# Kernel tuning notes

Measured on AMD Instinct MI355X. Metric: run time of the kernel, lower is better.

## Reference

```python
import jax, jax.numpy as jnp
import numpy as np

N_NODES = 100000
N_EDGES = 1600000
N_GRAPHS = 2000
IN_DIM = 37
HID = 128
OUT_CLS = 2


def _leconv(x, src, dst, w, W1, b1, W2, W3, b3):
    # PyG LEConv: out[i] = sum_j w_ij * (lin1(x)[i] - lin2(x)[j]) + lin3(x)[i]
    a = x @ W1 + b1          # [N, H]
    b = x @ W2               # [N, H] (lin2 has no bias)
    c = x @ W3 + b3          # [N, H]
    deg = jax.ops.segment_sum(w, dst, num_segments=N_NODES)              # [N]
    agg = jax.ops.segment_sum(w[:, None] * b[src], dst, num_segments=N_NODES)  # [N, H]
    return deg[:, None] * a - agg + c


def setup_inputs() -> dict:
    key = jax.random.key(0)
    ks = jax.random.split(key, 32)
    inp = {}
    inp["x"] = jax.random.normal(ks[0], (N_NODES, IN_DIM), dtype=jnp.float32)
    inp["edge_index"] = jax.random.randint(ks[1], (2, N_EDGES), 0, N_NODES, dtype=jnp.int64)
    inp["batch"] = jnp.sort(jax.random.randint(ks[2], (N_NODES,), 0, N_GRAPHS, dtype=jnp.int64))
    dims = [(IN_DIM, HID), (HID, HID), (HID, HID)]
    ki = 3
    for l, (di, do) in enumerate(dims):
        s = 1.0 / np.sqrt(di)
        inp[f"W1_{l}"] = jax.random.uniform(ks[ki + 0], (di, do), jnp.float32, -s, s)
        inp[f"b1_{l}"] = jax.random.uniform(ks[ki + 1], (do,), jnp.float32, -s, s)
        inp[f"W2_{l}"] = jax.random.uniform(ks[ki + 2], (di, do), jnp.float32, -s, s)
        inp[f"W3_{l}"] = jax.random.uniform(ks[ki + 3], (di, do), jnp.float32, -s, s)
        inp[f"b3_{l}"] = jax.random.uniform(ks[ki + 4], (do,), jnp.float32, -s, s)
        ki += 5
    sf = 1.0 / np.sqrt(HID)
    inp["Wf1"] = jax.random.uniform(ks[ki + 0], (HID, HID), jnp.float32, -sf, sf)
    inp["bf1"] = jax.random.uniform(ks[ki + 1], (HID,), jnp.float32, -sf, sf)
    inp["Wf2"] = jax.random.uniform(ks[ki + 2], (HID, OUT_CLS), jnp.float32, -sf, sf)
    inp["bf2"] = jax.random.uniform(ks[ki + 3], (OUT_CLS,), jnp.float32, -sf, sf)
    return inp


def reference(x, edge_index, batch,
              W1_0, b1_0, W2_0, W3_0, b3_0,
              W1_1, b1_1, W2_1, W3_1, b3_1,
              W1_2, b1_2, W2_2, W3_2, b3_2,
              Wf1, bf1, Wf2, bf2):
    src, dst = edge_index[0], edge_index[1]
    w = jnp.ones((edge_index.shape[1],), dtype=x.dtype)  # edge_weight = ones
    layers = [(W1_0, b1_0, W2_0, W3_0, b3_0),
              (W1_1, b1_1, W2_1, W3_1, b3_1),
              (W1_2, b1_2, W2_2, W3_2, b3_2)]
    h = x
    for (W1, b1, W2, W3, b3) in layers:
        h = jax.nn.relu(_leconv(h, src, dst, w, W1, b1, W2, W3, b3))
    # global mean pool per graph
    sums = jax.ops.segment_sum(h, batch, num_segments=N_GRAPHS)           # [G, H]
    cnt = jax.ops.segment_sum(jnp.ones((N_NODES,), h.dtype), batch, num_segments=N_GRAPHS)
    graph_x = sums / jnp.clip(cnt, 1.0)[:, None]
    # FFN head (Dropout is identity at inference)
    pred = jax.nn.relu(graph_x @ Wf1 + bf1) @ Wf2 + bf2                   # [G, 2]
    return pred
```

## Files before the change

### kernel.cpp

```cpp
#include <hip/hip_runtime.h>
#include <hip/hip_bf16.h>
#include <cstdint>

#define N_NODES 100000
#define N_EDGES 1600000
#define N_GRAPHS 2000
#define IN_DIM 37
#define HID 128

#define GEMM_GRID 1563
#define HIST_BLOCKS 6250
#define PACK67_BLOCKS 384
#define PREPACK_BLOCKS 96

typedef __attribute__((ext_vector_type(8))) short short8;
typedef __attribute__((ext_vector_type(4))) float f32x4;

static __device__ __forceinline__ short bf16_bits(float f) {
    __hip_bfloat16 h = __float2bfloat16(f);
    return *reinterpret_cast<short*>(&h);
}
static __device__ __forceinline__ float bf16_lo(uint32_t u) {
    uint32_t v = u << 16;
    return *reinterpret_cast<float*>(&v);
}
static __device__ __forceinline__ float bf16_hi(uint32_t u) {
    uint32_t v = u & 0xffff0000u;
    return *reinterpret_cast<float*>(&v);
}
static __device__ __forceinline__ uint32_t pack_bf16(float lo, float hi) {
    return ((uint32_t)(uint16_t)bf16_bits(hi) << 16) | (uint16_t)bf16_bits(lo);
}


struct PackArgs {
    const float* w[9];
    short* o[9];
};

static __device__ __forceinline__ void pack_one(const PackArgs& pa, int m, int r, int kin) {
    const int i = r & 7, lane = (r >> 3) & 63, t = (r >> 9) & 7, kb = r >> 12;
    const int k = kb * 32 + (lane >> 4) * 8 + i;
    const int c = t * 16 + (lane & 15);
    float v = (k < kin) ? pa.w[m][(size_t)k * HID + c] : 0.f;
    pa.o[m][r] = bf16_bits(v);
}

__global__ __launch_bounds__(256) void prepack_kernel(PackArgs pa) {
    const int idx = blockIdx.x * 256 + threadIdx.x;
    pack_one(pa, idx >> 13, idx & 8191, IN_DIM);
}


static __device__ __forceinline__ void gemm0_body(
    int blk, const float* __restrict__ x,
    const short* __restrict__ Wp1, const short* __restrict__ Wp2, const short* __restrict__ Wp3,
    const float* __restrict__ b1v, const float* __restrict__ b3v,
    short* __restrict__ D0, short* __restrict__ E0, short* __restrict__ Bb) {
    const int tid = threadIdx.x;
    const int wave = tid >> 6, lane = tid & 63;
    const int row_base = blk * 64 + wave * 16;
    const int r15 = lane & 15, kg = lane >> 4;
    int arow = row_base + r15;
    if (arow >= N_NODES) arow = N_NODES - 1;
    const float* xr = x + (size_t)arow * IN_DIM;

    f32x4 acc1[8], acc2[8], acc3[8];
    #pragma unroll
    for (int t = 0; t < 8; t++) {
        acc1[t] = (f32x4)0.f; acc2[t] = (f32x4)0.f; acc3[t] = (f32x4)0.f;
    }
    #pragma unroll
    for (int kb = 0; kb < 2; kb++) {
        short8 av;
        #pragma unroll
        for (int i = 0; i < 8; i++) {
            const int k = kb * 32 + kg * 8 + i;
            av[i] = (k < IN_DIM) ? bf16_bits(xr[k]) : (short)0;
        }
        #pragma unroll
        for (int t = 0; t < 8; t++) {
            const int widx = (kb * 8 + t) * 512 + lane * 8;
            short8 w1 = *(const short8*)(Wp1 + widx);
            short8 w2 = *(const short8*)(Wp2 + widx);
            short8 w3 = *(const short8*)(Wp3 + widx);
            acc1[t] = __builtin_amdgcn_mfma_f32_16x16x32_bf16(av, w1, acc1[t], 0, 0, 0);
            acc2[t] = __builtin_amdgcn_mfma_f32_16x16x32_bf16(av, w2, acc2[t], 0, 0, 0);
            acc3[t] = __builtin_amdgcn_mfma_f32_16x16x32_bf16(av, w3, acc3[t], 0, 0, 0);
        }
    }
    int grow[4]; bool ok[4];
    #pragma unroll
    for (int i = 0; i < 4; i++) {
        grow[i] = row_base + kg * 4 + i;
        ok[i] = grow[i] < N_NODES;
    }
    #pragma unroll
    for (int t = 0; t < 8; t++) {
        const int c = t * 16 + r15;
        const float bb1 = b1v[c], bb3 = b3v[c];
        #pragma unroll
        for (int i = 0; i < 4; i++) {
            if (ok[i]) {
                size_t o = (size_t)grow[i] * HID + c;
                D0[o] = bf16_bits(acc1[t][i] + bb1);
                E0[o] = bf16_bits(acc3[t][i] + bb3);
                Bb[o] = bf16_bits(acc2[t][i]);
            }
        }
    }
}


struct P1Args {
    const float* x;
    const int* ei;
    int* cnt; int* rank;
    const short* Wp1; const short* Wp2; const short* Wp3;
    const float* b1; const float* b3;
    short* D0; short* E0; short* Bb;
    PackArgs pa;
};

__global__ __launch_bounds__(256) void phase1_kernel(P1Args a) {
    const int b = blockIdx.x;
    if (b < GEMM_GRID) {
        gemm0_body(b, a.x, a.Wp1, a.Wp2, a.Wp3, a.b1, a.b3, a.D0, a.E0, a.Bb);
        return;
    }
    if (b < GEMM_GRID + HIST_BLOCKS) {
        const int e = (b - GEMM_GRID) * 256 + threadIdx.x;
        const int d = a.ei[N_EDGES + e];
        a.rank[e] = atomicAdd(&a.cnt[d], 1);
        return;
    }
    const int idx = (b - GEMM_GRID - HIST_BLOCKS) * 256 + threadIdx.x;
    pack_one(a.pa, 3 + (idx >> 14), idx & 16383, HID);
}


__global__ __launch_bounds__(1024) void scan_blocks(const int* __restrict__ cnt,
                                                    int* __restrict__ partial,
                                                    int* __restrict__ bsum) {
    __shared__ int ws[16];
    const int tid = threadIdx.x, lane = tid & 63, wv = tid >> 6;
    const int i = blockIdx.x * 1024 + tid;
    int v0 = (i < N_NODES) ? cnt[i] : 0;
    int v = v0;
    #pragma unroll
    for (int off = 1; off < 64; off <<= 1) {
        int n = __shfl_up(v, off, 64);
        if (lane >= off) v += n;
    }
    if (lane == 63) ws[wv] = v;
    __syncthreads();
    int woff = 0, tot = 0;
    #pragma unroll
    for (int w = 0; w < 16; w++) {
        int s = ws[w];
        if (w < wv) woff += s;
        tot += s;
    }
    if (i < N_NODES) partial[i] = woff + v - v0;
    if (tid == 0) bsum[blockIdx.x] = tot;
}

__global__ __launch_bounds__(1024) void scan_finalize(const int* __restrict__ partial,
                                                      const int* __restrict__ bsum,
                                                      const int* __restrict__ cnt,
                                                      int* __restrict__ rowptr,
                                                      float* __restrict__ degf) {
    __shared__ int off_s;
    const int tid = threadIdx.x, b = blockIdx.x;
    if (tid < 64) {
        int acc = 0;
        for (int j = tid; j < b; j += 64) acc += bsum[j];
        #pragma unroll
        for (int off = 32; off; off >>= 1) acc += __shfl_down(acc, off, 64);
        if (tid == 0) off_s = acc;
    }
    __syncthreads();
    const int i = b * 1024 + tid;
    if (i < N_NODES) {
        rowptr[i] = off_s + partial[i];
        degf[i] = (float)cnt[i];
    }
    if (b == 0 && tid == 0) rowptr[N_NODES] = N_EDGES;
}


__global__ __launch_bounds__(256) void fill_kernel(const int* __restrict__ ei,
                                                   const int* __restrict__ rank,
                                                   const int* __restrict__ rowptr,
                                                   int* __restrict__ col) {
    const int e = blockIdx.x * 256 + threadIdx.x;
    const int s = ei[e];
    const int d = ei[N_EDGES + e];
    col[rowptr[d] + rank[e]] = s;
}


static __device__ __forceinline__ void agg_edges4(const int* __restrict__ col, int s, int e,
                                                  const short* __restrict__ Bb,
                                                  int lane, int grp, int l16, float* acc) {
    for (int base = s; base < e; base += 64) {
        const int cnt = min(64, e - base);
        const int ci = base + lane;
        const int cv = col[(ci < e) ? ci : (e - 1)];
        for (int t = 0; t < cnt; t += 4) {
            const int idx = t + grp;
            const bool on = idx < cnt;
            const float w = on ? 1.f : 0.f;
            const int c = __shfl(cv, on ? idx : 0, 64);
            const uint4 u = *(const uint4*)(Bb + (size_t)c * HID + l16 * 8);
            acc[0] = fmaf(w, bf16_lo(u.x), acc[0]);
            acc[1] = fmaf(w, bf16_hi(u.x), acc[1]);
            acc[2] = fmaf(w, bf16_lo(u.y), acc[2]);
            acc[3] = fmaf(w, bf16_hi(u.y), acc[3]);
            acc[4] = fmaf(w, bf16_lo(u.z), acc[4]);
            acc[5] = fmaf(w, bf16_hi(u.z), acc[5]);
            acc[6] = fmaf(w, bf16_lo(u.w), acc[6]);
            acc[7] = fmaf(w, bf16_hi(u.w), acc[7]);
        }
    }
    #pragma unroll
    for (int j = 0; j < 8; j++) {
        acc[j] += __shfl_xor(acc[j], 16, 64);
        acc[j] += __shfl_xor(acc[j], 32, 64);
    }
}

__global__ __launch_bounds__(256) void gather0_kernel(const int* __restrict__ rowptr,
                                                      const int* __restrict__ col,
                                                      const short* __restrict__ Bb,
                                                      const short* __restrict__ D0,
                                                      const short* __restrict__ E0,
                                                      short* __restrict__ Hb) {
    const int wid = (blockIdx.x * 256 + threadIdx.x) >> 6;
    if (wid >= N_NODES) return;
    const int lane = threadIdx.x & 63, grp = lane >> 4, l16 = lane & 15;
    const int s = rowptr[wid], e = rowptr[wid + 1];
    float acc[8] = {0.f, 0.f, 0.f, 0.f, 0.f, 0.f, 0.f, 0.f};
    agg_edges4(col, s, e, Bb, lane, grp, l16, acc);
    if (grp == 0) {
        const float dg = (float)(e - s);
        const uint4 ud = *(const uint4*)(D0 + (size_t)wid * HID + l16 * 8);
        const uint4 ue = *(const uint4*)(E0 + (size_t)wid * HID + l16 * 8);
        uint4 r;
        r.x = pack_bf16(fmaxf(fmaf(dg, bf16_lo(ud.x), bf16_lo(ue.x)) - acc[0], 0.f),
                        fmaxf(fmaf(dg, bf16_hi(ud.x), bf16_hi(ue.x)) - acc[1], 0.f));
        r.y = pack_bf16(fmaxf(fmaf(dg, bf16_lo(ud.y), bf16_lo(ue.y)) - acc[2], 0.f),
                        fmaxf(fmaf(dg, bf16_hi(ud.y), bf16_hi(ue.y)) - acc[3], 0.f));
        r.z = pack_bf16(fmaxf(fmaf(dg, bf16_lo(ud.z), bf16_lo(ue.z)) - acc[4], 0.f),
                        fmaxf(fmaf(dg, bf16_hi(ud.z), bf16_hi(ue.z)) - acc[5], 0.f));
        r.w = pack_bf16(fmaxf(fmaf(dg, bf16_lo(ud.w), bf16_lo(ue.w)) - acc[6], 0.f),
                        fmaxf(fmaf(dg, bf16_hi(ud.w), bf16_hi(ue.w)) - acc[7], 0.f));
        *(uint4*)(Hb + (size_t)wid * HID + l16 * 8) = r;
    }
}

__global__ __launch_bounds__(256) void gatherL_kernel(const int* __restrict__ rowptr,
                                                      const int* __restrict__ col,
                                                      const short* __restrict__ Bb,
                                                      const short* __restrict__ OUTb,
                                                      short* __restrict__ Hb) {
    const int wid = (blockIdx.x * 256 + threadIdx.x) >> 6;
    if (wid >= N_NODES) return;
    const int lane = threadIdx.x & 63, grp = lane >> 4, l16 = lane & 15;
    const int s = rowptr[wid], e = rowptr[wid + 1];
    float acc[8] = {0.f, 0.f, 0.f, 0.f, 0.f, 0.f, 0.f, 0.f};
    agg_edges4(col, s, e, Bb, lane, grp, l16, acc);
    if (grp == 0) {
        const uint4 uo = *(const uint4*)(OUTb + (size_t)wid * HID + l16 * 8);
        uint4 r;
        r.x = pack_bf16(fmaxf(bf16_lo(uo.x) - acc[0], 0.f), fmaxf(bf16_hi(uo.x) - acc[1], 0.f));
        r.y = pack_bf16(fmaxf(bf16_lo(uo.y) - acc[2], 0.f), fmaxf(bf16_hi(uo.y) - acc[3], 0.f));
        r.z = pack_bf16(fmaxf(bf16_lo(uo.z) - acc[4], 0.f), fmaxf(bf16_hi(uo.z) - acc[5], 0.f));
        r.w = pack_bf16(fmaxf(bf16_lo(uo.w) - acc[6], 0.f), fmaxf(bf16_hi(uo.w) - acc[7], 0.f));
        *(uint4*)(Hb + (size_t)wid * HID + l16 * 8) = r;
    }
}


__global__ __launch_bounds__(256) void leconv_mfma(
    const short* __restrict__ Hb,
    const short* __restrict__ Wp1, const short* __restrict__ Wp2, const short* __restrict__ Wp3,
    const float* __restrict__ b1v, const float* __restrict__ b3v,
    const float* __restrict__ deg,
    short* __restrict__ Bb, short* __restrict__ OUTb) {
    const int tid = threadIdx.x;
    const int wave = tid >> 6, lane = tid & 63;
    const int row_base = blockIdx.x * 64 + wave * 16;
    const int r15 = lane & 15, kg = lane >> 4;
    int arow = row_base + r15;
    if (arow >= N_NODES) arow = N_NODES - 1;
    const short* aptr = Hb + (size_t)arow * HID + kg * 8;

    f32x4 acc1[8], acc2[8], acc3[8];
    #pragma unroll
    for (int t = 0; t < 8; t++) {
        acc1[t] = (f32x4)0.f; acc2[t] = (f32x4)0.f; acc3[t] = (f32x4)0.f;
    }
    #pragma unroll
    for (int kb = 0; kb < 4; kb++) {
        short8 av = *(const short8*)(aptr + kb * 32);
        #pragma unroll
        for (int t = 0; t < 8; t++) {
            const int widx = (kb * 8 + t) * 512 + lane * 8;
            short8 w1 = *(const short8*)(Wp1 + widx);
            short8 w2 = *(const short8*)(Wp2 + widx);
            short8 w3 = *(const short8*)(Wp3 + widx);
            acc1[t] = __builtin_amdgcn_mfma_f32_16x16x32_bf16(av, w1, acc1[t], 0, 0, 0);
            acc2[t] = __builtin_amdgcn_mfma_f32_16x16x32_bf16(av, w2, acc2[t], 0, 0, 0);
            acc3[t] = __builtin_amdgcn_mfma_f32_16x16x32_bf16(av, w3, acc3[t], 0, 0, 0);
        }
    }
    int grow[4]; bool ok[4]; float dg[4];
    #pragma unroll
    for (int i = 0; i < 4; i++) {
        grow[i] = row_base + kg * 4 + i;
        ok[i] = grow[i] < N_NODES;
        dg[i] = ok[i] ? deg[grow[i]] : 0.f;
    }
    #pragma unroll
    for (int t = 0; t < 8; t++) {
        const int c = t * 16 + r15;
        const float bb1 = b1v[c], bb3 = b3v[c];
        #pragma unroll
        for (int i = 0; i < 4; i++) {
            if (ok[i]) {
                size_t o = (size_t)grow[i] * HID + c;
                OUTb[o] = bf16_bits(dg[i] * (acc1[t][i] + bb1) + acc3[t][i] + bb3);
                Bb[o] = bf16_bits(acc2[t][i]);
            }
        }
    }
}


__global__ __launch_bounds__(128) void pool_ffn_kernel(const short* __restrict__ H,
                                                       const int* __restrict__ batch,
                                                       const float* __restrict__ Wf1,
                                                       const float* __restrict__ bf1,
                                                       const float* __restrict__ Wf2,
                                                       const float* __restrict__ bf2,
                                                       float* __restrict__ out) {
    const int g = blockIdx.x;
    const int t = threadIdx.x;

    int lo = 0, hi = N_NODES;
    while (lo < hi) { int mid = (lo + hi) >> 1; if (batch[mid] < g) lo = mid + 1; else hi = mid; }
    const int s = lo;
    hi = N_NODES;
    while (lo < hi) { int mid = (lo + hi) >> 1; if (batch[mid] < g + 1) lo = mid + 1; else hi = mid; }
    const int e = lo;

    float sum = 0.f;
    for (int n = s; n < e; n++) {
        short b = H[(size_t)n * HID + t];
        sum += __bfloat162float(*(__hip_bfloat16*)&b);
    }
    const float cntf = (float)(e - s);
    const float gx = sum / fmaxf(cntf, 1.f);

    __shared__ float lds[HID];
    lds[t] = gx;
    __syncthreads();

    float hsum = bf1[t];
    #pragma unroll 8
    for (int k = 0; k < HID; k++) hsum = fmaf(lds[k], Wf1[k * HID + t], hsum);
    const float hr = fmaxf(hsum, 0.f);

    float p0 = hr * Wf2[t * 2 + 0];
    float p1 = hr * Wf2[t * 2 + 1];
    #pragma unroll
    for (int off = 32; off > 0; off >>= 1) {
        p0 += __shfl_down(p0, off, 64);
        p1 += __shfl_down(p1, off, 64);
    }
    __shared__ float red[4];
    if ((t & 63) == 0) {
        red[(t >> 6) * 2 + 0] = p0;
        red[(t >> 6) * 2 + 1] = p1;
    }
    __syncthreads();
    if (t == 0) {
        out[g * 2 + 0] = red[0] + red[2] + bf2[0];
        out[g * 2 + 1] = red[1] + red[3] + bf2[1];
    }
}


extern "C" void kernel_launch(void* const* d_in, const int* in_sizes, int n_in,
                              void* d_out, int out_size, void* d_ws, size_t ws_size,
                              hipStream_t stream) {
    (void)in_sizes; (void)n_in; (void)out_size; (void)ws_size;

    const float* x     = (const float*)d_in[0];
    const int*   ei    = (const int*)d_in[1];
    const int*   batch = (const int*)d_in[2];
    const float* W[9] = {
        (const float*)d_in[3],  (const float*)d_in[5],  (const float*)d_in[6],
        (const float*)d_in[8],  (const float*)d_in[10], (const float*)d_in[11],
        (const float*)d_in[13], (const float*)d_in[15], (const float*)d_in[16]};
    const float* b1_0 = (const float*)d_in[4];
    const float* b3_0 = (const float*)d_in[7];
    const float* b1_1 = (const float*)d_in[9];
    const float* b3_1 = (const float*)d_in[12];
    const float* b1_2 = (const float*)d_in[14];
    const float* b3_2 = (const float*)d_in[17];
    const float* Wf1  = (const float*)d_in[18];
    const float* bf1  = (const float*)d_in[19];
    const float* Wf2  = (const float*)d_in[20];
    const float* bf2  = (const float*)d_in[21];
    float* out = (float*)d_out;

    char* ws = (char*)d_ws;
    size_t off = 0;
    auto alloc = [&](size_t bytes) {
        void* p = ws + off;
        off += (bytes + 255) & ~(size_t)255;
        return p;
    };
    short* D0     = (short*)alloc((size_t)N_NODES * HID * 2);
    short* E0     = (short*)alloc((size_t)N_NODES * HID * 2);
    short* Bb_A   = (short*)alloc((size_t)N_NODES * HID * 2);
    short* Bb_B   = (short*)alloc((size_t)N_NODES * HID * 2);
    short* Hb     = (short*)alloc((size_t)N_NODES * HID * 2);
    float* degf   = (float*)alloc((size_t)N_NODES * 4);
    int*   rowptr = (int*)alloc((size_t)(N_NODES + 1) * 4);
    int*   cnt    = (int*)alloc((size_t)N_NODES * 4);
    int*   col    = (int*)alloc((size_t)N_EDGES * 4);
    int*   rank   = (int*)alloc((size_t)N_EDGES * 4);
    int*   partial= (int*)alloc((size_t)N_NODES * 4);
    int*   bsum   = (int*)alloc(1024);
    short* P[9];
    for (int m = 0; m < 9; m++) P[m] = (short*)alloc(16384 * 2);

    hipMemsetAsync(cnt, 0, (size_t)N_NODES * 4, stream);

    PackArgs pa;
    for (int m = 0; m < 9; m++) { pa.w[m] = W[m]; pa.o[m] = P[m]; }

    prepack_kernel<<<PREPACK_BLOCKS, 256, 0, stream>>>(pa);

    P1Args p1{ x, ei, cnt, rank, P[0], P[1], P[2], b1_0, b3_0, D0, E0, Bb_A, pa };
    phase1_kernel<<<GEMM_GRID + HIST_BLOCKS + PACK67_BLOCKS, 256, 0, stream>>>(p1);

    const int NSB = (N_NODES + 1023) / 1024;
    scan_blocks<<<NSB, 1024, 0, stream>>>(cnt, partial, bsum);
    scan_finalize<<<NSB, 1024, 0, stream>>>(partial, bsum, cnt, rowptr, degf);

    fill_kernel<<<HIST_BLOCKS, 256, 0, stream>>>(ei, rank, rowptr, col);

    const int gather_grid = (N_NODES * 64 + 255) / 256;

    gather0_kernel<<<gather_grid, 256, 0, stream>>>(rowptr, col, Bb_A, D0, E0, Hb);
    leconv_mfma<<<GEMM_GRID, 256, 0, stream>>>(Hb, P[3], P[4], P[5], b1_1, b3_1, degf, Bb_B, E0);
    gatherL_kernel<<<gather_grid, 256, 0, stream>>>(rowptr, col, Bb_B, E0, Hb);
    leconv_mfma<<<GEMM_GRID, 256, 0, stream>>>(Hb, P[6], P[7], P[8], b1_2, b3_2, degf, Bb_A, D0);
    gatherL_kernel<<<gather_grid, 256, 0, stream>>>(rowptr, col, Bb_A, D0, Hb);

    pool_ffn_kernel<<<N_GRAPHS, 128, 0, stream>>>(Hb, batch, Wf1, bf1, Wf2, bf2, out);
}
```

Baseline: 475.3 us.

## Fuse final gather with mean-pool and FFN, merge prepack and transpose MFMA outputs

The last gatherL pass and the pool/FFN kernel become one per-graph kernel. Each graph's nodes are aggregated, passed through ReLU and summed in registers, so the final Hb write and re-read go away. The prepack is folded into the histogram kernel, and the layer-0 GEMM moves into the fill kernel, saving launches. MFMA operands are swapped so each lane holds 4 consecutive features of one node, which allows vectorized ushort4 stores and float4 bias loads. The cost is that the final gather now runs with only 2000 blocks sized by graph, which may leave the GPU underused or unbalanced.

```diff
diff --git a/kernel.cpp b/kernel.cpp
--- a/kernel.cpp
+++ b/kernel.cpp
@@ -10,8 +10,7 @@
 
 #define GEMM_GRID 1563
 #define HIST_BLOCKS 6250
-#define PACK67_BLOCKS 384
-#define PREPACK_BLOCKS 96
+#define PACK_BLOCKS 480
 
 typedef __attribute__((ext_vector_type(8))) short short8;
 typedef __attribute__((ext_vector_type(4))) float f32x4;
@@ -27,9 +26,6 @@
 static __device__ __forceinline__ float bf16_hi(uint32_t u) {
     uint32_t v = u & 0xffff0000u;
     return *reinterpret_cast<float*>(&v);
-}
-static __device__ __forceinline__ uint32_t pack_bf16(float lo, float hi) {
-    return ((uint32_t)(uint16_t)bf16_bits(hi) << 16) | (uint16_t)bf16_bits(lo);
 }
 
 
@@ -46,9 +42,71 @@
     pa.o[m][r] = bf16_bits(v);
 }
 
-__global__ __launch_bounds__(256) void prepack_kernel(PackArgs pa) {
-    const int idx = blockIdx.x * 256 + threadIdx.x;
-    pack_one(pa, idx >> 13, idx & 8191, IN_DIM);
+
+__global__ __launch_bounds__(256) void phase1_kernel(const int* __restrict__ ei,
+                                                     int* __restrict__ cnt,
+                                                     int* __restrict__ rank,
+                                                     PackArgs pa) {
+    const int b = blockIdx.x;
+    if (b < HIST_BLOCKS) {
+        const int e = b * 256 + threadIdx.x;
+        const int d = ei[N_EDGES + e];
+        rank[e] = atomicAdd(&cnt[d], 1);
+        return;
+    }
+    const int idx = (b - HIST_BLOCKS) * 256 + threadIdx.x;
+    if (idx < 24576) pack_one(pa, idx >> 13, idx & 8191, IN_DIM);
+    else { const int q = idx - 24576; pack_one(pa, 3 + (q >> 14), q & 16383, HID); }
+}
+
+
+__global__ __launch_bounds__(1024) void scan_blocks(const int* __restrict__ cnt,
+                                                    int* __restrict__ partial,
+                                                    int* __restrict__ bsum) {
+    __shared__ int ws[16];
+    const int tid = threadIdx.x, lane = tid & 63, wv = tid >> 6;
+    const int i = blockIdx.x * 1024 + tid;
+    int v0 = (i < N_NODES) ? cnt[i] : 0;
+    int v = v0;
+    #pragma unroll
+    for (int off = 1; off < 64; off <<= 1) {
+        int n = __shfl_up(v, off, 64);
+        if (lane >= off) v += n;
+    }
+    if (lane == 63) ws[wv] = v;
+    __syncthreads();
+    int woff = 0, tot = 0;
+    #pragma unroll
+    for (int w = 0; w < 16; w++) {
+        int s = ws[w];
+        if (w < wv) woff += s;
+        tot += s;
+    }
+    if (i < N_NODES) partial[i] = woff + v - v0;
+    if (tid == 0) bsum[blockIdx.x] = tot;
+}
+
+__global__ __launch_bounds__(1024) void scan_finalize(const int* __restrict__ partial,
+                                                      const int* __restrict__ bsum,
+                                                      const int* __restrict__ cnt,
+                                                      int* __restrict__ rowptr,
+                                                      float* __restrict__ degf) {
+    __shared__ int off_s;
+    const int tid = threadIdx.x, b = blockIdx.x;
+    if (tid < 64) {
+        int acc = 0;
+        for (int j = tid; j < b; j += 64) acc += bsum[j];
+        #pragma unroll
+        for (int off = 32; off; off >>= 1) acc += __shfl_down(acc, off, 64);
+        if (tid == 0) off_s = acc;
+    }
+    __syncthreads();
+    const int i = b * 1024 + tid;
+    if (i < N_NODES) {
+        rowptr[i] = off_s + partial[i];
+        degf[i] = (float)cnt[i];
+    }
+    if (b == 0 && tid == 0) rowptr[N_NODES] = N_EDGES;
 }
 
 
@@ -84,119 +142,55 @@
             short8 w1 = *(const short8*)(Wp1 + widx);
             short8 w2 = *(const short8*)(Wp2 + widx);
             short8 w3 = *(const short8*)(Wp3 + widx);
-            acc1[t] = __builtin_amdgcn_mfma_f32_16x16x32_bf16(av, w1, acc1[t], 0, 0, 0);
-            acc2[t] = __builtin_amdgcn_mfma_f32_16x16x32_bf16(av, w2, acc2[t], 0, 0, 0);
-            acc3[t] = __builtin_amdgcn_mfma_f32_16x16x32_bf16(av, w3, acc3[t], 0, 0, 0);
-        }
-    }
-    int grow[4]; bool ok[4];
-    #pragma unroll
-    for (int i = 0; i < 4; i++) {
-        grow[i] = row_base + kg * 4 + i;
-        ok[i] = grow[i] < N_NODES;
-    }
-    #pragma unroll
-    for (int t = 0; t < 8; t++) {
-        const int c = t * 16 + r15;
-        const float bb1 = b1v[c], bb3 = b3v[c];
-        #pragma unroll
-        for (int i = 0; i < 4; i++) {
-            if (ok[i]) {
-                size_t o = (size_t)grow[i] * HID + c;
-                D0[o] = bf16_bits(acc1[t][i] + bb1);
-                E0[o] = bf16_bits(acc3[t][i] + bb3);
-                Bb[o] = bf16_bits(acc2[t][i]);
-            }
-        }
-    }
-}
-
-
-struct P1Args {
-    const float* x;
-    const int* ei;
-    int* cnt; int* rank;
-    const short* Wp1; const short* Wp2; const short* Wp3;
-    const float* b1; const float* b3;
-    short* D0; short* E0; short* Bb;
-    PackArgs pa;
-};
-
-__global__ __launch_bounds__(256) void phase1_kernel(P1Args a) {
+            acc1[t] = __builtin_amdgcn_mfma_f32_16x16x32_bf16(w1, av, acc1[t], 0, 0, 0);
+            acc2[t] = __builtin_amdgcn_mfma_f32_16x16x32_bf16(w2, av, acc2[t], 0, 0, 0);
+            acc3[t] = __builtin_amdgcn_mfma_f32_16x16x32_bf16(w3, av, acc3[t], 0, 0, 0);
+        }
+    }
+    const int node = row_base + r15;
+    if (node < N_NODES) {
+        #pragma unroll
+        for (int t = 0; t < 8; t++) {
+            const int f = t * 16 + kg * 4;
+            const float4 bb1 = *(const float4*)(b1v + f);
+            const float4 bb3 = *(const float4*)(b3v + f);
+            ushort4 od, oe, ob;
+            od.x = (unsigned short)bf16_bits(acc1[t][0] + bb1.x);
+            od.y = (unsigned short)bf16_bits(acc1[t][1] + bb1.y);
+            od.z = (unsigned short)bf16_bits(acc1[t][2] + bb1.z);
+            od.w = (unsigned short)bf16_bits(acc1[t][3] + bb1.w);
+            oe.x = (unsigned short)bf16_bits(acc3[t][0] + bb3.x);
+            oe.y = (unsigned short)bf16_bits(acc3[t][1] + bb3.y);
+            oe.z = (unsigned short)bf16_bits(acc3[t][2] + bb3.z);
+            oe.w = (unsigned short)bf16_bits(acc3[t][3] + bb3.w);
+            ob.x = (unsigned short)bf16_bits(acc2[t][0]);
+            ob.y = (unsigned short)bf16_bits(acc2[t][1]);
+            ob.z = (unsigned short)bf16_bits(acc2[t][2]);
+            ob.w = (unsigned short)bf16_bits(acc2[t][3]);
+            *(ushort4*)(D0 + (size_t)node * HID + f) = od;
+            *(ushort4*)(E0 + (size_t)node * HID + f) = oe;
+            *(ushort4*)(Bb + (size_t)node * HID + f) = ob;
+        }
+    }
+}
+
+
+__global__ __launch_bounds__(256) void fill_gemm0_kernel(
+    const int* __restrict__ ei, const int* __restrict__ rank, const int* __restrict__ rowptr,
+    int* __restrict__ col,
+    const float* __restrict__ x,
+    const short* __restrict__ Wp1, const short* __restrict__ Wp2, const short* __restrict__ Wp3,
+    const float* __restrict__ b1v, const float* __restrict__ b3v,
+    short* __restrict__ D0, short* __restrict__ E0, short* __restrict__ Bb) {
     const int b = blockIdx.x;
-    if (b < GEMM_GRID) {
-        gemm0_body(b, a.x, a.Wp1, a.Wp2, a.Wp3, a.b1, a.b3, a.D0, a.E0, a.Bb);
+    if (b < HIST_BLOCKS) {
+        const int e = b * 256 + threadIdx.x;
+        const int s = ei[e];
+        const int d = ei[N_EDGES + e];
+        col[rowptr[d] + rank[e]] = s;
         return;
     }
-    if (b < GEMM_GRID + HIST_BLOCKS) {
-        const int e = (b - GEMM_GRID) * 256 + threadIdx.x;
-        const int d = a.ei[N_EDGES + e];
-        a.rank[e] = atomicAdd(&a.cnt[d], 1);
-        return;
-    }
-    const int idx = (b - GEMM_GRID - HIST_BLOCKS) * 256 + threadIdx.x;
-    pack_one(a.pa, 3 + (idx >> 14), idx & 16383, HID);
-}
-
-
-__global__ __launch_bounds__(1024) void scan_blocks(const int* __restrict__ cnt,
-                                                    int* __restrict__ partial,
-                                                    int* __restrict__ bsum) {
-    __shared__ int ws[16];
-    const int tid = threadIdx.x, lane = tid & 63, wv = tid >> 6;
-    const int i = blockIdx.x * 1024 + tid;
-    int v0 = (i < N_NODES) ? cnt[i] : 0;
-    int v = v0;
-    #pragma unroll
-    for (int off = 1; off < 64; off <<= 1) {
-        int n = __shfl_up(v, off, 64);
-        if (lane >= off) v += n;
-    }
-    if (lane == 63) ws[wv] = v;
-    __syncthreads();
-    int woff = 0, tot = 0;
-    #pragma unroll
-    for (int w = 0; w < 16; w++) {
-        int s = ws[w];
-        if (w < wv) woff += s;
-        tot += s;
-    }
-    if (i < N_NODES) partial[i] = woff + v - v0;
-    if (tid == 0) bsum[blockIdx.x] = tot;
-}
-
-__global__ __launch_bounds__(1024) void scan_finalize(const int* __restrict__ partial,
-                                                      const int* __restrict__ bsum,
-                                                      const int* __restrict__ cnt,
-                                                      int* __restrict__ rowptr,
-                                                      float* __restrict__ degf) {
-    __shared__ int off_s;
-    const int tid = threadIdx.x, b = blockIdx.x;
-    if (tid < 64) {
-        int acc = 0;
-        for (int j = tid; j < b; j += 64) acc += bsum[j];
-        #pragma unroll
-        for (int off = 32; off; off >>= 1) acc += __shfl_down(acc, off, 64);
-        if (tid == 0) off_s = acc;
-    }
-    __syncthreads();
-    const int i = b * 1024 + tid;
-    if (i < N_NODES) {
-        rowptr[i] = off_s + partial[i];
-        degf[i] = (float)cnt[i];
-    }
-    if (b == 0 && tid == 0) rowptr[N_NODES] = N_EDGES;
-}
-
-
-__global__ __launch_bounds__(256) void fill_kernel(const int* __restrict__ ei,
-                                                   const int* __restrict__ rank,
-                                                   const int* __restrict__ rowptr,
-                                                   int* __restrict__ col) {
-    const int e = blockIdx.x * 256 + threadIdx.x;
-    const int s = ei[e];
-    const int d = ei[N_EDGES + e];
-    col[rowptr[d] + rank[e]] = s;
+    gemm0_body(b - HIST_BLOCKS, x, Wp1, Wp2, Wp3, b1v, b3v, D0, E0, Bb);
 }
 
 
@@ -228,6 +222,10 @@
         acc[j] += __shfl_xor(acc[j], 16, 64);
         acc[j] += __shfl_xor(acc[j], 32, 64);
     }
+}
+
+static __device__ __forceinline__ uint32_t pack_bf16(float lo, float hi) {
+    return ((uint32_t)(uint16_t)bf16_bits(hi) << 16) | (uint16_t)bf16_bits(lo);
 }
 
 __global__ __launch_bounds__(256) void gather0_kernel(const int* __restrict__ rowptr,
@@ -286,7 +284,7 @@
     const short* __restrict__ Hb,
     const short* __restrict__ Wp1, const short* __restrict__ Wp2, const short* __restrict__ Wp3,
     const float* __restrict__ b1v, const float* __restrict__ b3v,
-    const float* __restrict__ deg,
+    const float* __restrict__ degf,
     short* __restrict__ Bb, short* __restrict__ OUTb) {
     const int tid = threadIdx.x;
     const int wave = tid >> 6, lane = tid & 63;
@@ -310,43 +308,45 @@
             short8 w1 = *(const short8*)(Wp1 + widx);
             short8 w2 = *(const short8*)(Wp2 + widx);
             short8 w3 = *(const short8*)(Wp3 + widx);
-            acc1[t] = __builtin_amdgcn_mfma_f32_16x16x32_bf16(av, w1, acc1[t], 0, 0, 0);
-            acc2[t] = __builtin_amdgcn_mfma_f32_16x16x32_bf16(av, w2, acc2[t], 0, 0, 0);
-            acc3[t] = __builtin_amdgcn_mfma_f32_16x16x32_bf16(av, w3, acc3[t], 0, 0, 0);
-        }
-    }
-    int grow[4]; bool ok[4]; float dg[4];
-    #pragma unroll
-    for (int i = 0; i < 4; i++) {
-        grow[i] = row_base + kg * 4 + i;
-        ok[i] = grow[i] < N_NODES;
-        dg[i] = ok[i] ? deg[grow[i]] : 0.f;
-    }
-    #pragma unroll
-    for (int t = 0; t < 8; t++) {
-        const int c = t * 16 + r15;
-        const float bb1 = b1v[c], bb3 = b3v[c];
-        #pragma unroll
-        for (int i = 0; i < 4; i++) {
-            if (ok[i]) {
-                size_t o = (size_t)grow[i] * HID + c;
-                OUTb[o] = bf16_bits(dg[i] * (acc1[t][i] + bb1) + acc3[t][i] + bb3);
-                Bb[o] = bf16_bits(acc2[t][i]);
-            }
-        }
-    }
-}
-
-
-__global__ __launch_bounds__(128) void pool_ffn_kernel(const short* __restrict__ H,
-                                                       const int* __restrict__ batch,
-                                                       const float* __restrict__ Wf1,
-                                                       const float* __restrict__ bf1,
-                                                       const float* __restrict__ Wf2,
-                                                       const float* __restrict__ bf2,
-                                                       float* __restrict__ out) {
+            acc1[t] = __builtin_amdgcn_mfma_f32_16x16x32_bf16(w1, av, acc1[t], 0, 0, 0);
+            acc2[t] = __builtin_amdgcn_mfma_f32_16x16x32_bf16(w2, av, acc2[t], 0, 0, 0);
+            acc3[t] = __builtin_amdgcn_mfma_f32_16x16x32_bf16(w3, av, acc3[t], 0, 0, 0);
+        }
+    }
+    const int node = row_base + r15;
+    if (node < N_NODES) {
+        const float dg = degf[node];
+        #pragma unroll
+        for (int t = 0; t < 8; t++) {
+            const int f = t * 16 + kg * 4;
+            const float4 bb1 = *(const float4*)(b1v + f);
+            const float4 bb3 = *(const float4*)(b3v + f);
+            ushort4 oo, ob;
+            oo.x = (unsigned short)bf16_bits(dg * (acc1[t][0] + bb1.x) + acc3[t][0] + bb3.x);
+            oo.y = (unsigned short)bf16_bits(dg * (acc1[t][1] + bb1.y) + acc3[t][1] + bb3.y);
+            oo.z = (unsigned short)bf16_bits(dg * (acc1[t][2] + bb1.z) + acc3[t][2] + bb3.z);
+            oo.w = (unsigned short)bf16_bits(dg * (acc1[t][3] + bb1.w) + acc3[t][3] + bb3.w);
+            ob.x = (unsigned short)bf16_bits(acc2[t][0]);
+            ob.y = (unsigned short)bf16_bits(acc2[t][1]);
+            ob.z = (unsigned short)bf16_bits(acc2[t][2]);
+            ob.w = (unsigned short)bf16_bits(acc2[t][3]);
+            *(ushort4*)(OUTb + (size_t)node * HID + f) = oo;
+            *(ushort4*)(Bb + (size_t)node * HID + f) = ob;
+        }
+    }
+}
+
+
+__global__ __launch_bounds__(256) void gather_pool_ffn(
+    const int* __restrict__ rowptr, const int* __restrict__ col,
+    const short* __restrict__ Bb, const short* __restrict__ OUTb,
+    const int* __restrict__ batch,
+    const float* __restrict__ Wf1, const float* __restrict__ bf1,
+    const float* __restrict__ Wf2, const float* __restrict__ bf2,
+    float* __restrict__ out) {
     const int g = blockIdx.x;
-    const int t = threadIdx.x;
+    const int tid = threadIdx.x;
+    const int wave = tid >> 6, lane = tid & 63, grp = lane >> 4, l16 = lane & 15;
 
     int lo = 0, hi = N_NODES;
     while (lo < hi) { int mid = (lo + hi) >> 1; if (batch[mid] < g) lo = mid + 1; else hi = mid; }
@@ -355,37 +355,60 @@
     while (lo < hi) { int mid = (lo + hi) >> 1; if (batch[mid] < g + 1) lo = mid + 1; else hi = mid; }
     const int e = lo;
 
-    float sum = 0.f;
-    for (int n = s; n < e; n++) {
-        short b = H[(size_t)n * HID + t];
-        sum += __bfloat162float(*(__hip_bfloat16*)&b);
-    }
-    const float cntf = (float)(e - s);
-    const float gx = sum / fmaxf(cntf, 1.f);
-
-    __shared__ float lds[HID];
-    lds[t] = gx;
+    float msum[8] = {0.f, 0.f, 0.f, 0.f, 0.f, 0.f, 0.f, 0.f};
+    for (int node = s + wave; node < e; node += 4) {
+        const int s0 = rowptr[node], e0 = rowptr[node + 1];
+        float acc[8] = {0.f, 0.f, 0.f, 0.f, 0.f, 0.f, 0.f, 0.f};
+        agg_edges4(col, s0, e0, Bb, lane, grp, l16, acc);
+        if (grp == 0) {
+            const uint4 uo = *(const uint4*)(OUTb + (size_t)node * HID + l16 * 8);
+            msum[0] += fmaxf(bf16_lo(uo.x) - acc[0], 0.f);
+            msum[1] += fmaxf(bf16_hi(uo.x) - acc[1], 0.f);
+            msum[2] += fmaxf(bf16_lo(uo.y) - acc[2], 0.f);
+            msum[3] += fmaxf(bf16_hi(uo.y) - acc[3], 0.f);
+            msum[4] += fmaxf(bf16_lo(uo.z) - acc[4], 0.f);
+            msum[5] += fmaxf(bf16_hi(uo.z) - acc[5], 0.f);
+            msum[6] += fmaxf(bf16_lo(uo.w) - acc[6], 0.f);
+            msum[7] += fmaxf(bf16_hi(uo.w) - acc[7], 0.f);
+        }
+    }
+
+    __shared__ float smem[4][HID];
+    if (grp == 0) {
+        #pragma unroll
+        for (int j = 0; j < 8; j++) smem[wave][l16 * 8 + j] = msum[j];
+    }
     __syncthreads();
 
-    float hsum = bf1[t];
-    #pragma unroll 8
-    for (int k = 0; k < HID; k++) hsum = fmaf(lds[k], Wf1[k * HID + t], hsum);
-    const float hr = fmaxf(hsum, 0.f);
-
-    float p0 = hr * Wf2[t * 2 + 0];
-    float p1 = hr * Wf2[t * 2 + 1];
+    __shared__ float plds[HID];
+    if (tid < HID) {
+        const float gx = (smem[0][tid] + smem[1][tid] + smem[2][tid] + smem[3][tid]) /
+                         fmaxf((float)(e - s), 1.f);
+        plds[tid] = gx;
+    }
+    __syncthreads();
+
+    float p0 = 0.f, p1 = 0.f;
+    if (tid < HID) {
+        float hsum = bf1[tid];
+        #pragma unroll 8
+        for (int k = 0; k < HID; k++) hsum = fmaf(plds[k], Wf1[k * HID + tid], hsum);
+        const float hr = fmaxf(hsum, 0.f);
+        p0 = hr * Wf2[tid * 2 + 0];
+        p1 = hr * Wf2[tid * 2 + 1];
+    }
     #pragma unroll
     for (int off = 32; off > 0; off >>= 1) {
         p0 += __shfl_down(p0, off, 64);
         p1 += __shfl_down(p1, off, 64);
     }
     __shared__ float red[4];
-    if ((t & 63) == 0) {
-        red[(t >> 6) * 2 + 0] = p0;
-        red[(t >> 6) * 2 + 1] = p1;
+    if ((tid & 63) == 0 && tid < HID) {
+        red[(tid >> 6) * 2 + 0] = p0;
+        red[(tid >> 6) * 2 + 1] = p1;
     }
     __syncthreads();
-    if (t == 0) {
+    if (tid == 0) {
         out[g * 2 + 0] = red[0] + red[2] + bf2[0];
         out[g * 2 + 1] = red[1] + red[3] + bf2[1];
     }
@@ -443,16 +466,14 @@
     PackArgs pa;
     for (int m = 0; m < 9; m++) { pa.w[m] = W[m]; pa.o[m] = P[m]; }
 
-    prepack_kernel<<<PREPACK_BLOCKS, 256, 0, stream>>>(pa);
-
-    P1Args p1{ x, ei, cnt, rank, P[0], P[1], P[2], b1_0, b3_0, D0, E0, Bb_A, pa };
-    phase1_kernel<<<GEMM_GRID + HIST_BLOCKS + PACK67_BLOCKS, 256, 0, stream>>>(p1);
+    phase1_kernel<<<HIST_BLOCKS + PACK_BLOCKS, 256, 0, stream>>>(ei, cnt, rank, pa);
 
     const int NSB = (N_NODES + 1023) / 1024;
     scan_blocks<<<NSB, 1024, 0, stream>>>(cnt, partial, bsum);
     scan_finalize<<<NSB, 1024, 0, stream>>>(partial, bsum, cnt, rowptr, degf);
 
-    fill_kernel<<<HIST_BLOCKS, 256, 0, stream>>>(ei, rank, rowptr, col);
+    fill_gemm0_kernel<<<HIST_BLOCKS + GEMM_GRID, 256, 0, stream>>>(
+        ei, rank, rowptr, col, x, P[0], P[1], P[2], b1_0, b3_0, D0, E0, Bb_A);
 
     const int gather_grid = (N_NODES * 64 + 255) / 256;
 
@@ -460,7 +481,5 @@
     leconv_mfma<<<GEMM_GRID, 256, 0, stream>>>(Hb, P[3], P[4], P[5], b1_1, b3_1, degf, Bb_B, E0);
     gatherL_kernel<<<gather_grid, 256, 0, stream>>>(rowptr, col, Bb_B, E0, Hb);
     leconv_mfma<<<GEMM_GRID, 256, 0, stream>>>(Hb, P[6], P[7], P[8], b1_2, b3_2, degf, Bb_A, D0);
-    gatherL_kernel<<<gather_grid, 256, 0, stream>>>(rowptr, col, Bb_A, D0, Hb);
-
-    pool_ffn_kernel<<<N_GRAPHS, 128, 0, stream>>>(Hb, batch, Wf1, bf1, Wf2, bf2, out);
-}
+    gather_pool_ffn<<<N_GRAPHS, 256, 0, stream>>>(rowptr, col, Bb_A, D0, batch, Wf1, bf1, Wf2, bf2, out);
+}
```

Result: no change. 484.5 us (+1.9%).
